# Kernel optimization log

Hardware: AMD Instinct MI355X
Metric: run time of the kernel (lower is better)

Reference implementation:

```python
import jax, jax.numpy as jnp
import numpy as np


def setup_inputs() -> dict:
    key = jax.random.key(0)
    k1, k2 = jax.random.split(key)
    return {
        "embeddings": jax.random.normal(k1, (4, 768, 32, 32), dtype=jnp.float32),
        "database": jax.random.normal(k2, (20000, 768), dtype=jnp.float32),
        "k": 3,
        "out_h": 512,
        "out_w": 512,
    }


def reference(embeddings, database, k, out_h, out_w):
    # embeddings: [B, D, h, w]  (segmenter hidden state), database: [N, D]
    B, D, h, w = embeddings.shape
    # B x h x w x D -> B x (h*w) x D query layout, as in _get_ood_scores
    q = jnp.transpose(embeddings, (0, 2, 3, 1)).reshape(B, h * w, D)
    # squared Euclidean distances via (||q||^2 + ||x||^2 - 2 q.x)
    q2 = jnp.sum(q * q, axis=-1)[..., None]                 # [B, hw, 1]
    x2 = jnp.sum(database * database, axis=-1)[None, None]  # [1, 1, N]
    d2 = q2 + x2 - 2.0 * jnp.einsum("bqd,nd->bqn", q, database)
    dist = jnp.sqrt(jnp.maximum(d2, 1e-12))                 # [B, hw, N]
    # k smallest distances (sklearn kneighbors) then mean over neighbors
    neg_topk, _ = jax.lax.top_k(-dist, k)                   # [B, hw, k]
    ood = jnp.mean(-neg_topk, axis=-1).reshape(B, h, w)
    # F.interpolate(..., mode='bilinear', align_corners=False) == half-pixel bilinear
    ood_up = jax.image.resize(ood[:, None], (B, 1, out_h, out_w), method="bilinear")
    return ood_up
```

## Files before the change

### kernel.cpp

```cpp
#include <hip/hip_runtime.h>
#include <hip/hip_bf16.h>
#include <math.h>

constexpr int B    = 4;
constexpr int D    = 768;
constexpr int HW   = 1024;
constexpr int M    = B * HW;
constexpr int NDB  = 20000;
constexpr int LTP  = 160;
constexpr int OUTH = 512;
constexpr int OUTW = 512;

constexpr int BM     = 512;
constexpr int BN     = 128;
constexpr int KSTEPS = D / 64;
constexpr int NSPLIT = 8;
constexpr int NT     = 40;
constexpr int STEPB  = 128 * 64;

typedef int   i32x8  __attribute__((ext_vector_type(8)));
typedef float f32x16 __attribute__((ext_vector_type(16)));

__device__ __forceinline__ void insert3(float& t0, float& t1, float& t2, float d) {
    float a0 = fminf(d, t0);
    float b0 = fmaxf(d, t0);
    float a1 = fminf(b0, t1);
    float b1 = fmaxf(b0, t1);
    t0 = a0; t1 = a1;
    t2 = fminf(b1, t2);
}

__device__ __forceinline__ unsigned int pack4_fp8(float a, float b, float c, float d) {
    int v = __builtin_amdgcn_cvt_pk_fp8_f32(a, b, 0, false);
    v = __builtin_amdgcn_cvt_pk_fp8_f32(c, d, v, true);
    return (unsigned int)v;
}

__device__ __forceinline__ void gl_lds16(const unsigned char* g, unsigned char* l) {
    __builtin_amdgcn_global_load_lds(
        (const __attribute__((address_space(1))) void*)g,
        (__attribute__((address_space(3))) void*)l, 16, 0, 0);
}

__global__ __launch_bounds__(256) void db_convert(const float* __restrict__ db,
                                                  uint4* __restrict__ dbt8,
                                                  float* __restrict__ x2p) {
    __shared__ float panel[128][68];
    __shared__ float part[512];
    const int lt = blockIdx.x;
    const int g  = blockIdx.y;
    const int t  = threadIdx.x;
    const int n0 = lt * 128;

    #pragma unroll
    for (int pass = 0; pass < 8; ++pass) {
        int idx = pass * 256 + t;
        int row = idx >> 4, c4 = idx & 15;
        int n = n0 + row;
        float4 v = make_float4(0.f, 0.f, 0.f, 0.f);
        if (n < NDB) v = *(const float4*)(db + (size_t)n * D + g * 64 + c4 * 4);
        *(float4*)&panel[row][c4 * 4] = v;
    }
    __syncthreads();
    #pragma unroll
    for (int pass = 0; pass < 2; ++pass) {
        int idx = pass * 256 + t;
        int r  = idx & 31;
        int kc = (idx >> 5) & 1;
        int h2 = (idx >> 6) & 1;
        int rg = idx >> 7;
        int row  = rg * 32 + r;
        int kloc = kc * 32 + h2 * 16;
        float4 va = *(const float4*)&panel[row][kloc + 0];
        float4 vb = *(const float4*)&panel[row][kloc + 4];
        float4 vc = *(const float4*)&panel[row][kloc + 8];
        float4 vd = *(const float4*)&panel[row][kloc + 12];
        float ss = va.x*va.x + va.y*va.y + va.z*va.z + va.w*va.w
                 + vb.x*vb.x + vb.y*vb.y + vb.z*vb.z + vb.w*vb.w
                 + vc.x*vc.x + vc.y*vc.y + vc.z*vc.z + vc.w*vc.w
                 + vd.x*vd.x + vd.y*vd.y + vd.z*vd.z + vd.w*vd.w;
        uint4 o;
        o.x = pack4_fp8(va.x, va.y, va.z, va.w);
        o.y = pack4_fp8(vb.x, vb.y, vb.z, vb.w);
        o.z = pack4_fp8(vc.x, vc.y, vc.z, vc.w);
        o.w = pack4_fp8(vd.x, vd.y, vd.z, vd.w);
        dbt8[((size_t)lt * KSTEPS + g) * 512 + idx] = o;
        part[idx] = ss;
    }
    __syncthreads();
    if (t < 128) {
        int base = (t >> 5) * 128 + (t & 31);
        float s = part[base] + part[base + 32] + part[base + 64] + part[base + 96];
        x2p[((size_t)lt * KSTEPS + g) * 128 + t] = s;
    }
}

__global__ __launch_bounds__(256) void q_convert(const float* __restrict__ emb,
                                                 uint4* __restrict__ qbt8,
                                                 float* __restrict__ q2p) {
    __shared__ float part[512];
    const int qt = blockIdx.x;
    const int g  = blockIdx.y;
    const int t  = threadIdx.x;
    const int b  = qt >> 3;
    const int p0 = (qt & 7) * 128;

    #pragma unroll
    for (int pass = 0; pass < 2; ++pass) {
        int idx = pass * 256 + t;
        int r  = idx & 31;
        int kc = (idx >> 5) & 1;
        int h2 = (idx >> 6) & 1;
        int rg = idx >> 7;
        int prow = rg * 32 + r;
        int kb = g * 64 + kc * 32 + h2 * 16;
        const float* src = emb + ((size_t)b * D + kb) * HW + p0 + prow;
        float v[16];
        float ss = 0.f;
        #pragma unroll
        for (int j = 0; j < 16; ++j) {
            v[j] = src[(size_t)j * HW];
            ss = fmaf(v[j], v[j], ss);
        }
        uint4 o;
        o.x = pack4_fp8(-2.f*v[0],  -2.f*v[1],  -2.f*v[2],  -2.f*v[3]);
        o.y = pack4_fp8(-2.f*v[4],  -2.f*v[5],  -2.f*v[6],  -2.f*v[7]);
        o.z = pack4_fp8(-2.f*v[8],  -2.f*v[9],  -2.f*v[10], -2.f*v[11]);
        o.w = pack4_fp8(-2.f*v[12], -2.f*v[13], -2.f*v[14], -2.f*v[15]);
        qbt8[((size_t)qt * KSTEPS + g) * 512 + idx] = o;
        part[idx] = ss;
    }
    __syncthreads();
    if (t < 128) {
        int base = (t >> 5) * 128 + (t & 31);
        float s = part[base] + part[base + 32] + part[base + 64] + part[base + 96];
        q2p[((size_t)qt * KSTEPS + g) * 128 + t] = s;
    }
}

__global__ __launch_bounds__(512, 2) void gemm_topk(const unsigned char* __restrict__ dbt8,
                                                    const unsigned char* __restrict__ qbt8,
                                                    const float* __restrict__ x2p,
                                                    float* __restrict__ partials) {
    __shared__ __align__(16) unsigned char Bq[KSTEPS * 8192];
    __shared__ float red[8][BN][3];

    const int tid  = threadIdx.x;
    const int lane = tid & 63;
    const int w    = tid >> 6;
    const int h    = lane >> 5;
    const int l31  = lane & 31;

    const int bid   = blockIdx.x;
    const int sp    = bid & 7;
    const int qtile = bid >> 3;
    const int m0    = qtile * BN;

    {
        const unsigned char* qb = qbt8 + (size_t)qtile * KSTEPS * STEPB;
        #pragma unroll
        for (int p = 0; p < 12; ++p) {
            int idx = p * 512 + tid;
            gl_lds16(qb + (size_t)idx * 16, Bq + idx * 16);
        }
    }
    __syncthreads();

    int b_off[4];
    #pragma unroll
    for (int j4 = 0; j4 < 4; ++j4) b_off[j4] = j4 * 2048 + h * 512 + l31 * 16;

    float t0[4], t1[4], t2[4];
    #pragma unroll
    for (int j4 = 0; j4 < 4; ++j4) { t0[j4] = INFINITY; t1[j4] = INFINITY; t2[j4] = INFINITY; }

    const unsigned char* aP = dbt8 + ((size_t)(4 * sp + (w >> 1)) * KSTEPS) * STEPB
                              + (w & 1) * 4096 + h * 512 + l31 * 16;

    auto ldA = [&](i32x8& x0, i32x8& x1, const unsigned char* p) {
        int4 a = *(const int4*)(p);
        int4 b = *(const int4*)(p + 1024);
        int4 c = *(const int4*)(p + 2048);
        int4 d = *(const int4*)(p + 3072);
        x0 = (i32x8){a.x, a.y, a.z, a.w, b.x, b.y, b.z, b.w};
        x1 = (i32x8){c.x, c.y, c.z, c.w, d.x, d.y, d.z, d.w};
    };

    for (int t = sp; t < NT; t += NSPLIT) {
        float sx = 1e30f;
        {
            int n = t * 512 + w * 64 + lane;
            if (n < NDB) {
                const float* p = x2p + (size_t)(n >> 7) * (KSTEPS * 128) + (n & 127);
                sx = 0.f;
                #pragma unroll
                for (int g = 0; g < KSTEPS; ++g) sx += p[g * 128];
            }
        }

        f32x16 acc[2][4];
        #pragma unroll
        for (int i = 0; i < 2; ++i)
            #pragma unroll
            for (int j4 = 0; j4 < 4; ++j4)
                #pragma unroll
                for (int r = 0; r < 16; ++r) acc[i][j4][r] = 0.f;

        i32x8 af0, af1, an0, an1;
        const unsigned char* aPtr = aP;
        ldA(af0, af1, aPtr); aPtr += STEPB;
        #pragma unroll
        for (int g = 0; g < KSTEPS; ++g) {
            if (g + 1 < KSTEPS) { ldA(an0, an1, aPtr); aPtr += STEPB; }
            const unsigned char* Bb = Bq + g * 8192;
            i32x8 bf[4];
            #pragma unroll
            for (int j4 = 0; j4 < 4; ++j4) {
                int4 lo = *(const int4*)(Bb + b_off[j4]);
                int4 hi = *(const int4*)(Bb + b_off[j4] + 1024);
                bf[j4] = (i32x8){lo.x, lo.y, lo.z, lo.w, hi.x, hi.y, hi.z, hi.w};
            }
            __builtin_amdgcn_s_setprio(1);
            #pragma unroll
            for (int j4 = 0; j4 < 4; ++j4) {
                acc[0][j4] = __builtin_amdgcn_mfma_scale_f32_32x32x64_f8f6f4(
                    af0, bf[j4], acc[0][j4], 0, 0, 0, 0x7f7f7f7f, 0, 0x7f7f7f7f);
                acc[1][j4] = __builtin_amdgcn_mfma_scale_f32_32x32x64_f8f6f4(
                    af1, bf[j4], acc[1][j4], 0, 0, 0, 0x7f7f7f7f, 0, 0x7f7f7f7f);
            }
            __builtin_amdgcn_s_setprio(0);
            af0 = an0; af1 = an1;
        }
        aP += (size_t)32 * KSTEPS * STEPB;

        #pragma unroll
        for (int i = 0; i < 2; ++i) {
            #pragma unroll
            for (int rg2 = 0; rg2 < 4; ++rg2) {
                #pragma unroll
                for (int rr = 0; rr < 4; ++rr) {
                    float xv = __shfl(sx, i * 32 + rg2 * 8 + 4 * h + rr);
                    #pragma unroll
                    for (int j4 = 0; j4 < 4; ++j4)
                        insert3(t0[j4], t1[j4], t2[j4], acc[i][j4][rg2 * 4 + rr] + xv);
                }
            }
        }
    }

    #pragma unroll
    for (int j4 = 0; j4 < 4; ++j4) {
        float o0 = __shfl_xor(t0[j4], 32);
        float o1 = __shfl_xor(t1[j4], 32);
        float o2 = __shfl_xor(t2[j4], 32);
        insert3(t0[j4], t1[j4], t2[j4], o0);
        insert3(t0[j4], t1[j4], t2[j4], o1);
        insert3(t0[j4], t1[j4], t2[j4], o2);
    }
    if (h == 0) {
        #pragma unroll
        for (int j4 = 0; j4 < 4; ++j4) {
            int col = j4 * 32 + l31;
            red[w][col][0] = t0[j4];
            red[w][col][1] = t1[j4];
            red[w][col][2] = t2[j4];
        }
    }
    __syncthreads();
    if (tid < BN) {
        float a0 = red[0][tid][0], a1 = red[0][tid][1], a2 = red[0][tid][2];
        #pragma unroll
        for (int ww = 1; ww < 8; ++ww) {
            insert3(a0, a1, a2, red[ww][tid][0]);
            insert3(a0, a1, a2, red[ww][tid][1]);
            insert3(a0, a1, a2, red[ww][tid][2]);
        }
        float* dst = partials + ((size_t)(m0 + tid) * NSPLIT + sp) * 3;
        dst[0] = a0; dst[1] = a1; dst[2] = a2;
    }
}

__global__ __launch_bounds__(256) void merge_ood(const float* __restrict__ partials,
                                                 const float* __restrict__ q2p,
                                                 float* __restrict__ ood) {
    int m = blockIdx.x * 256 + threadIdx.x;
    if (m >= M) return;
    const float* pp = partials + (size_t)m * NSPLIT * 3;
    float a0 = INFINITY, a1 = INFINITY, a2 = INFINITY;
    #pragma unroll
    for (int j = 0; j < NSPLIT * 3; ++j) insert3(a0, a1, a2, pp[j]);
    const float* qp = q2p + (size_t)(m >> 7) * KSTEPS * 128 + (m & 127);
    float q = 0.f;
    #pragma unroll
    for (int g = 0; g < KSTEPS; ++g) q += qp[g * 128];
    float d0 = sqrtf(fmaxf(q + a0, 1e-12f));
    float d1 = sqrtf(fmaxf(q + a1, 1e-12f));
    float d2 = sqrtf(fmaxf(q + a2, 1e-12f));
    ood[m] = (d0 + d1 + d2) * (1.f / 3.f);
}

__global__ __launch_bounds__(256) void upsample(const float* __restrict__ ood,
                                                float* __restrict__ out) {
    int idx = blockIdx.x * 256 + threadIdx.x;
    int ox = idx & (OUTW - 1);
    int oy = (idx >> 9) & (OUTH - 1);
    int bb = idx >> 18;
    float sx = (ox + 0.5f) * (32.f / OUTW) - 0.5f;
    float sy = (oy + 0.5f) * (32.f / OUTH) - 0.5f;
    float fx = floorf(sx), fy = floorf(sy);
    float wx = sx - fx, wy = sy - fy;
    int x0 = max(0, min(31, (int)fx));
    int x1 = max(0, min(31, (int)fx + 1));
    int y0 = max(0, min(31, (int)fy));
    int y1 = max(0, min(31, (int)fy + 1));
    const float* src = ood + bb * 1024;
    float v00 = src[y0 * 32 + x0];
    float v01 = src[y0 * 32 + x1];
    float v10 = src[y1 * 32 + x0];
    float v11 = src[y1 * 32 + x1];
    float top = v00 + wx * (v01 - v00);
    float bot = v10 + wx * (v11 - v10);
    out[idx] = top + wy * (bot - top);
}

extern "C" void kernel_launch(void* const* d_in, const int* in_sizes, int n_in,
                              void* d_out, int out_size, void* d_ws, size_t ws_size,
                              hipStream_t stream) {
    const float* emb = (const float*)d_in[0];
    const float* db  = (const float*)d_in[1];
    float* out = (float*)d_out;

    char* ws = (char*)d_ws;
    unsigned char* dbt8 = (unsigned char*)ws;
    unsigned char* qbt8 = (unsigned char*)(ws + 15728640);
    float* x2p      = (float*)(ws + 18874368);
    float* q2p      = (float*)(ws + 19857408);
    float* ood      = (float*)(ws + 20054016);
    float* partials = (float*)(ws + 20070400);

    db_convert<<<dim3(LTP, KSTEPS), 256, 0, stream>>>(db, (uint4*)dbt8, x2p);
    q_convert<<<dim3(32, KSTEPS), 256, 0, stream>>>(emb, (uint4*)qbt8, q2p);
    gemm_topk<<<NSPLIT * 32, 512, 0, stream>>>(dbt8, qbt8, x2p, partials);
    merge_ood<<<(M + 255) / 256, 256, 0, stream>>>(partials, q2p, ood);
    upsample<<<(B * OUTH * OUTW) / 256, 256, 0, stream>>>(ood, out);
}
```

Baseline: 219.8 us.

## Halve GEMM block size, double split count, and triple-buffer query tiles in LDS

The fused distance GEMM/top-k kernel now uses 256-thread blocks over 256-row database tiles with 16 splits, which doubles the grid to 512 blocks. Blocks are mapped so each XCD handles one split. The full 96 KB query tile is no longer preloaded into LDS. Query K-slices are now streamed through a 3-slot ring buffer with async global-to-LDS loads, with explicit waitcnt/barrier staging interleaved between the MFMA halves. Database tiling is changed to 158 tiles with uneven per-split tile counts. The aim is to raise occupancy, cut LDS footprint and overlap loads with compute, at the cost of many more barriers per K-step.

```diff
diff --git a/kernel.cpp b/kernel.cpp
--- a/kernel.cpp
+++ b/kernel.cpp
@@ -7,15 +7,15 @@
 constexpr int HW   = 1024;
 constexpr int M    = B * HW;
 constexpr int NDB  = 20000;
-constexpr int LTP  = 160;
+constexpr int LT   = 158;
 constexpr int OUTH = 512;
 constexpr int OUTW = 512;
 
-constexpr int BM     = 512;
+constexpr int BM     = 256;
 constexpr int BN     = 128;
 constexpr int KSTEPS = D / 64;
-constexpr int NSPLIT = 8;
-constexpr int NT     = 40;
+constexpr int NSPLIT = 16;
+constexpr int NT2    = 79;
 constexpr int STEPB  = 128 * 64;
 
 typedef int   i32x8  __attribute__((ext_vector_type(8)));
@@ -138,44 +138,38 @@
     }
 }
 
-__global__ __launch_bounds__(512, 2) void gemm_topk(const unsigned char* __restrict__ dbt8,
+__global__ __launch_bounds__(256, 2) void gemm_topk(const unsigned char* __restrict__ dbt8,
                                                     const unsigned char* __restrict__ qbt8,
                                                     const float* __restrict__ x2p,
                                                     float* __restrict__ partials) {
-    __shared__ __align__(16) unsigned char Bq[KSTEPS * 8192];
-    __shared__ float red[8][BN][3];
+    __shared__ __align__(16) unsigned char Bsm[3 * 8192];
+    __shared__ float red[4][BN][3];
 
     const int tid  = threadIdx.x;
     const int lane = tid & 63;
     const int w    = tid >> 6;
+    const int lts  = w >> 1;
+    const int wr   = w & 1;
     const int h    = lane >> 5;
     const int l31  = lane & 31;
 
     const int bid   = blockIdx.x;
-    const int sp    = bid & 7;
-    const int qtile = bid >> 3;
+    const int xcd   = bid & 7;
+    const int j     = bid >> 3;
+    const int sp    = xcd + 8 * (j >> 5);
+    const int qtile = j & 31;
     const int m0    = qtile * BN;
 
-    {
-        const unsigned char* qb = qbt8 + (size_t)qtile * KSTEPS * STEPB;
-        #pragma unroll
-        for (int p = 0; p < 12; ++p) {
-            int idx = p * 512 + tid;
-            gl_lds16(qb + (size_t)idx * 16, Bq + idx * 16);
-        }
-    }
-    __syncthreads();
-
     int b_off[4];
     #pragma unroll
     for (int j4 = 0; j4 < 4; ++j4) b_off[j4] = j4 * 2048 + h * 512 + l31 * 16;
 
-    float t0[4], t1[4], t2[4];
-    #pragma unroll
-    for (int j4 = 0; j4 < 4; ++j4) { t0[j4] = INFINITY; t1[j4] = INFINITY; t2[j4] = INFINITY; }
-
-    const unsigned char* aP = dbt8 + ((size_t)(4 * sp + (w >> 1)) * KSTEPS) * STEPB
-                              + (w & 1) * 4096 + h * 512 + l31 * 16;
+    const int frag = wr * 4096 + h * 512 + l31 * 16;
+
+    const unsigned char* bQ = qbt8 + (size_t)qtile * KSTEPS * STEPB + w * 2048 + lane * 16;
+    unsigned char* bD = Bsm + w * 2048;
+
+    const int ntiles = (sp <= 14) ? 5 : 4;
 
     auto ldA = [&](i32x8& x0, i32x8& x1, const unsigned char* p) {
         int4 a = *(const int4*)(p);
@@ -185,18 +179,42 @@
         x0 = (i32x8){a.x, a.y, a.z, a.w, b.x, b.y, b.z, b.w};
         x1 = (i32x8){c.x, c.y, c.z, c.w, d.x, d.y, d.z, d.w};
     };
-
-    for (int t = sp; t < NT; t += NSPLIT) {
-        float sx = 1e30f;
-        {
-            int n = t * 512 + w * 64 + lane;
-            if (n < NDB) {
-                const float* p = x2p + (size_t)(n >> 7) * (KSTEPS * 128) + (n & 127);
-                sx = 0.f;
-                #pragma unroll
-                for (int g = 0; g < KSTEPS; ++g) sx += p[g * 128];
-            }
-        }
+    auto ldB = [&](i32x8& f, const unsigned char* Bb, int off) {
+        int4 lo = *(const int4*)(Bb + off);
+        int4 hi = *(const int4*)(Bb + off + 1024);
+        f = (i32x8){lo.x, lo.y, lo.z, lo.w, hi.x, hi.y, hi.z, hi.w};
+    };
+
+    gl_lds16(bQ + 0 * STEPB,        bD + 0 * 8192);
+    gl_lds16(bQ + 0 * STEPB + 1024, bD + 0 * 8192 + 1024);
+    const unsigned char* aT = dbt8 + (size_t)(2 * sp + lts) * KSTEPS * STEPB + frag;
+    i32x8 af0, af1, an0, an1;
+    ldA(af0, af1, aT);
+    gl_lds16(bQ + 1 * STEPB,        bD + 1 * 8192);
+    gl_lds16(bQ + 1 * STEPB + 1024, bD + 1 * 8192 + 1024);
+    asm volatile("s_waitcnt vmcnt(6)" ::: "memory");
+    __builtin_amdgcn_sched_barrier(0);
+    __builtin_amdgcn_s_barrier();
+    __builtin_amdgcn_sched_barrier(0);
+
+    float sx = 1e30f;
+    {
+        int n = sp * BM + w * 64 + lane;
+        if (n < NDB) {
+            const float* p = x2p + (size_t)(n >> 7) * (KSTEPS * 128) + (n & 127);
+            sx = 0.f;
+            #pragma unroll
+            for (int g = 0; g < KSTEPS; ++g) sx += p[g * 128];
+        }
+    }
+
+    float t0[4], t1[4], t2[4];
+    #pragma unroll
+    for (int j4 = 0; j4 < 4; ++j4) { t0[j4] = INFINITY; t1[j4] = INFINITY; t2[j4] = INFINITY; }
+
+    for (int tt = 0; tt < ntiles; ++tt) {
+        const unsigned char* aTn = (tt + 1 < ntiles)
+            ? aT + (size_t)2 * NSPLIT * KSTEPS * STEPB : aT;
 
         f32x16 acc[2][4];
         #pragma unroll
@@ -206,32 +224,57 @@
                 #pragma unroll
                 for (int r = 0; r < 16; ++r) acc[i][j4][r] = 0.f;
 
-        i32x8 af0, af1, an0, an1;
-        const unsigned char* aPtr = aP;
-        ldA(af0, af1, aPtr); aPtr += STEPB;
         #pragma unroll
         for (int g = 0; g < KSTEPS; ++g) {
-            if (g + 1 < KSTEPS) { ldA(an0, an1, aPtr); aPtr += STEPB; }
-            const unsigned char* Bb = Bq + g * 8192;
-            i32x8 bf[4];
-            #pragma unroll
-            for (int j4 = 0; j4 < 4; ++j4) {
-                int4 lo = *(const int4*)(Bb + b_off[j4]);
-                int4 hi = *(const int4*)(Bb + b_off[j4] + 1024);
-                bf[j4] = (i32x8){lo.x, lo.y, lo.z, lo.w, hi.x, hi.y, hi.z, hi.w};
-            }
+            const unsigned char* Bb = Bsm + (g % 3) * 8192;
+            const int sb = ((g + 2) % 3) * 8192;
+            const int gs = (g + 2) % KSTEPS;
+
+            i32x8 bf0, bf1;
+            ldB(bf0, Bb, b_off[0]);
+            ldB(bf1, Bb, b_off[1]);
+            { const unsigned char* aLd = (g < KSTEPS - 1) ? (aT + (g + 1) * STEPB) : aTn;
+              ldA(an0, an1, aLd); }
+            asm volatile("s_waitcnt vmcnt(6)" ::: "memory");
+            __builtin_amdgcn_sched_barrier(0);
+            __builtin_amdgcn_s_barrier();
+            __builtin_amdgcn_sched_barrier(0);
+            asm volatile("s_waitcnt lgkmcnt(0)" ::: "memory");
             __builtin_amdgcn_s_setprio(1);
-            #pragma unroll
-            for (int j4 = 0; j4 < 4; ++j4) {
-                acc[0][j4] = __builtin_amdgcn_mfma_scale_f32_32x32x64_f8f6f4(
-                    af0, bf[j4], acc[0][j4], 0, 0, 0, 0x7f7f7f7f, 0, 0x7f7f7f7f);
-                acc[1][j4] = __builtin_amdgcn_mfma_scale_f32_32x32x64_f8f6f4(
-                    af1, bf[j4], acc[1][j4], 0, 0, 0, 0x7f7f7f7f, 0, 0x7f7f7f7f);
-            }
+            acc[0][0] = __builtin_amdgcn_mfma_scale_f32_32x32x64_f8f6f4(
+                af0, bf0, acc[0][0], 0, 0, 0, 0x7f7f7f7f, 0, 0x7f7f7f7f);
+            acc[1][0] = __builtin_amdgcn_mfma_scale_f32_32x32x64_f8f6f4(
+                af1, bf0, acc[1][0], 0, 0, 0, 0x7f7f7f7f, 0, 0x7f7f7f7f);
+            acc[0][1] = __builtin_amdgcn_mfma_scale_f32_32x32x64_f8f6f4(
+                af0, bf1, acc[0][1], 0, 0, 0, 0x7f7f7f7f, 0, 0x7f7f7f7f);
+            acc[1][1] = __builtin_amdgcn_mfma_scale_f32_32x32x64_f8f6f4(
+                af1, bf1, acc[1][1], 0, 0, 0, 0x7f7f7f7f, 0, 0x7f7f7f7f);
             __builtin_amdgcn_s_setprio(0);
+
+            i32x8 bf2, bf3;
+            ldB(bf2, Bb, b_off[2]);
+            ldB(bf3, Bb, b_off[3]);
+            gl_lds16(bQ + gs * STEPB,        bD + sb);
+            gl_lds16(bQ + gs * STEPB + 1024, bD + sb + 1024);
+            asm volatile("s_waitcnt vmcnt(6)" ::: "memory");
+            __builtin_amdgcn_sched_barrier(0);
+            __builtin_amdgcn_s_barrier();
+            __builtin_amdgcn_sched_barrier(0);
+            asm volatile("s_waitcnt lgkmcnt(0)" ::: "memory");
+            __builtin_amdgcn_s_setprio(1);
+            acc[0][2] = __builtin_amdgcn_mfma_scale_f32_32x32x64_f8f6f4(
+                af0, bf2, acc[0][2], 0, 0, 0, 0x7f7f7f7f, 0, 0x7f7f7f7f);
+            acc[1][2] = __builtin_amdgcn_mfma_scale_f32_32x32x64_f8f6f4(
+                af1, bf2, acc[1][2], 0, 0, 0, 0x7f7f7f7f, 0, 0x7f7f7f7f);
+            acc[0][3] = __builtin_amdgcn_mfma_scale_f32_32x32x64_f8f6f4(
+                af0, bf3, acc[0][3], 0, 0, 0, 0x7f7f7f7f, 0, 0x7f7f7f7f);
+            acc[1][3] = __builtin_amdgcn_mfma_scale_f32_32x32x64_f8f6f4(
+                af1, bf3, acc[1][3], 0, 0, 0, 0x7f7f7f7f, 0, 0x7f7f7f7f);
+            __builtin_amdgcn_s_setprio(0);
+
             af0 = an0; af1 = an1;
         }
-        aP += (size_t)32 * KSTEPS * STEPB;
+        aT = aTn;
 
         #pragma unroll
         for (int i = 0; i < 2; ++i) {
@@ -246,6 +289,17 @@
                 }
             }
         }
+
+        if (tt + 1 < ntiles) {
+            int n = (sp + (tt + 1) * NSPLIT) * BM + w * 64 + lane;
+            sx = 1e30f;
+            if (n < NDB) {
+                const float* p = x2p + (size_t)(n >> 7) * (KSTEPS * 128) + (n & 127);
+                sx = 0.f;
+                #pragma unroll
+                for (int g = 0; g < KSTEPS; ++g) sx += p[g * 128];
+            }
+        }
     }
 
     #pragma unroll
@@ -270,7 +324,7 @@
     if (tid < BN) {
         float a0 = red[0][tid][0], a1 = red[0][tid][1], a2 = red[0][tid][2];
         #pragma unroll
-        for (int ww = 1; ww < 8; ++ww) {
+        for (int ww = 1; ww < 4; ++ww) {
             insert3(a0, a1, a2, red[ww][tid][0]);
             insert3(a0, a1, a2, red[ww][tid][1]);
             insert3(a0, a1, a2, red[ww][tid][2]);
@@ -332,15 +386,15 @@
 
     char* ws = (char*)d_ws;
     unsigned char* dbt8 = (unsigned char*)ws;
-    unsigned char* qbt8 = (unsigned char*)(ws + 15728640);
-    float* x2p      = (float*)(ws + 18874368);
-    float* q2p      = (float*)(ws + 19857408);
-    float* ood      = (float*)(ws + 20054016);
-    float* partials = (float*)(ws + 20070400);
-
-    db_convert<<<dim3(LTP, KSTEPS), 256, 0, stream>>>(db, (uint4*)dbt8, x2p);
+    unsigned char* qbt8 = (unsigned char*)(ws + 15532032);
+    float* x2p      = (float*)(ws + 18677760);
+    float* q2p      = (float*)(ws + 19648512);
+    float* ood      = (float*)(ws + 19845120);
+    float* partials = (float*)(ws + 19861504);
+
+    db_convert<<<dim3(LT, KSTEPS), 256, 0, stream>>>(db, (uint4*)dbt8, x2p);
     q_convert<<<dim3(32, KSTEPS), 256, 0, stream>>>(emb, (uint4*)qbt8, q2p);
-    gemm_topk<<<NSPLIT * 32, 512, 0, stream>>>(dbt8, qbt8, x2p, partials);
+    gemm_topk<<<NSPLIT * 32, 256, 0, stream>>>(dbt8, qbt8, x2p, partials);
     merge_ood<<<(M + 255) / 256, 256, 0, stream>>>(partials, q2p, ood);
     upsample<<<(B * OUTH * OUTW) / 256, 256, 0, stream>>>(ood, out);
 }
```

Result: slower. 793.0 us (+260.8%).

## Fuse conversion kernels and double-buffer query tiles in smaller GEMM blocks

Applied to the files above, without the earlier changes.

Merges the database and query fp8 conversion kernels into one launch. Reworks gemm_topk to use 256-thread blocks with a 256-row database tile and 16-way split, launching 512 blocks instead of 256 and mapping splits across XCDs. Instead of staging the whole 96KB query tile in LDS up front, it streams per-k-step query slices into a 16KB double buffer. This adds a barrier each k-step and drops the setprio hints. The intent is lower LDS use, better occupancy and less prologue latency, at the cost of more synchronisation and more query reloads.

```diff
diff --git a/kernel.cpp b/kernel.cpp
--- a/kernel.cpp
+++ b/kernel.cpp
@@ -7,15 +7,15 @@
 constexpr int HW   = 1024;
 constexpr int M    = B * HW;
 constexpr int NDB  = 20000;
-constexpr int LTP  = 160;
+constexpr int LT   = 158;
 constexpr int OUTH = 512;
 constexpr int OUTW = 512;
 
-constexpr int BM     = 512;
+constexpr int BM     = 256;
 constexpr int BN     = 128;
 constexpr int KSTEPS = D / 64;
-constexpr int NSPLIT = 8;
-constexpr int NT     = 40;
+constexpr int NSPLIT = 16;
+constexpr int NT2    = 79;
 constexpr int STEPB  = 128 * 64;
 
 typedef int   i32x8  __attribute__((ext_vector_type(8)));
@@ -42,140 +42,132 @@
         (__attribute__((address_space(3))) void*)l, 16, 0, 0);
 }
 
-__global__ __launch_bounds__(256) void db_convert(const float* __restrict__ db,
-                                                  uint4* __restrict__ dbt8,
-                                                  float* __restrict__ x2p) {
+__global__ __launch_bounds__(256) void convert_all(const float* __restrict__ db,
+                                                   const float* __restrict__ emb,
+                                                   uint4* __restrict__ dbt8,
+                                                   uint4* __restrict__ qbt8,
+                                                   float* __restrict__ x2p,
+                                                   float* __restrict__ q2p) {
     __shared__ float panel[128][68];
     __shared__ float part[512];
-    const int lt = blockIdx.x;
-    const int g  = blockIdx.y;
-    const int t  = threadIdx.x;
-    const int n0 = lt * 128;
-
-    #pragma unroll
-    for (int pass = 0; pass < 8; ++pass) {
-        int idx = pass * 256 + t;
-        int row = idx >> 4, c4 = idx & 15;
-        int n = n0 + row;
-        float4 v = make_float4(0.f, 0.f, 0.f, 0.f);
-        if (n < NDB) v = *(const float4*)(db + (size_t)n * D + g * 64 + c4 * 4);
-        *(float4*)&panel[row][c4 * 4] = v;
-    }
-    __syncthreads();
-    #pragma unroll
-    for (int pass = 0; pass < 2; ++pass) {
-        int idx = pass * 256 + t;
-        int r  = idx & 31;
-        int kc = (idx >> 5) & 1;
-        int h2 = (idx >> 6) & 1;
-        int rg = idx >> 7;
-        int row  = rg * 32 + r;
-        int kloc = kc * 32 + h2 * 16;
-        float4 va = *(const float4*)&panel[row][kloc + 0];
-        float4 vb = *(const float4*)&panel[row][kloc + 4];
-        float4 vc = *(const float4*)&panel[row][kloc + 8];
-        float4 vd = *(const float4*)&panel[row][kloc + 12];
-        float ss = va.x*va.x + va.y*va.y + va.z*va.z + va.w*va.w
-                 + vb.x*vb.x + vb.y*vb.y + vb.z*vb.z + vb.w*vb.w
-                 + vc.x*vc.x + vc.y*vc.y + vc.z*vc.z + vc.w*vc.w
-                 + vd.x*vd.x + vd.y*vd.y + vd.z*vd.z + vd.w*vd.w;
-        uint4 o;
-        o.x = pack4_fp8(va.x, va.y, va.z, va.w);
-        o.y = pack4_fp8(vb.x, vb.y, vb.z, vb.w);
-        o.z = pack4_fp8(vc.x, vc.y, vc.z, vc.w);
-        o.w = pack4_fp8(vd.x, vd.y, vd.z, vd.w);
-        dbt8[((size_t)lt * KSTEPS + g) * 512 + idx] = o;
-        part[idx] = ss;
-    }
-    __syncthreads();
-    if (t < 128) {
-        int base = (t >> 5) * 128 + (t & 31);
-        float s = part[base] + part[base + 32] + part[base + 64] + part[base + 96];
-        x2p[((size_t)lt * KSTEPS + g) * 128 + t] = s;
-    }
-}
-
-__global__ __launch_bounds__(256) void q_convert(const float* __restrict__ emb,
-                                                 uint4* __restrict__ qbt8,
-                                                 float* __restrict__ q2p) {
-    __shared__ float part[512];
-    const int qt = blockIdx.x;
-    const int g  = blockIdx.y;
-    const int t  = threadIdx.x;
-    const int b  = qt >> 3;
-    const int p0 = (qt & 7) * 128;
-
-    #pragma unroll
-    for (int pass = 0; pass < 2; ++pass) {
-        int idx = pass * 256 + t;
-        int r  = idx & 31;
-        int kc = (idx >> 5) & 1;
-        int h2 = (idx >> 6) & 1;
-        int rg = idx >> 7;
-        int prow = rg * 32 + r;
-        int kb = g * 64 + kc * 32 + h2 * 16;
-        const float* src = emb + ((size_t)b * D + kb) * HW + p0 + prow;
-        float v[16];
-        float ss = 0.f;
-        #pragma unroll
-        for (int j = 0; j < 16; ++j) {
-            v[j] = src[(size_t)j * HW];
-            ss = fmaf(v[j], v[j], ss);
-        }
-        uint4 o;
-        o.x = pack4_fp8(-2.f*v[0],  -2.f*v[1],  -2.f*v[2],  -2.f*v[3]);
-        o.y = pack4_fp8(-2.f*v[4],  -2.f*v[5],  -2.f*v[6],  -2.f*v[7]);
-        o.z = pack4_fp8(-2.f*v[8],  -2.f*v[9],  -2.f*v[10], -2.f*v[11]);
-        o.w = pack4_fp8(-2.f*v[12], -2.f*v[13], -2.f*v[14], -2.f*v[15]);
-        qbt8[((size_t)qt * KSTEPS + g) * 512 + idx] = o;
-        part[idx] = ss;
-    }
-    __syncthreads();
-    if (t < 128) {
-        int base = (t >> 5) * 128 + (t & 31);
-        float s = part[base] + part[base + 32] + part[base + 64] + part[base + 96];
-        q2p[((size_t)qt * KSTEPS + g) * 128 + t] = s;
-    }
-}
-
-__global__ __launch_bounds__(512, 2) void gemm_topk(const unsigned char* __restrict__ dbt8,
+    const int g = blockIdx.y;
+    const int t = threadIdx.x;
+
+    if (blockIdx.x < LT) {
+        const int lt = blockIdx.x;
+        const int n0 = lt * 128;
+
+        #pragma unroll
+        for (int pass = 0; pass < 8; ++pass) {
+            int idx = pass * 256 + t;
+            int row = idx >> 4, c4 = idx & 15;
+            int n = n0 + row;
+            float4 v = make_float4(0.f, 0.f, 0.f, 0.f);
+            if (n < NDB) v = *(const float4*)(db + (size_t)n * D + g * 64 + c4 * 4);
+            *(float4*)&panel[row][c4 * 4] = v;
+        }
+        __syncthreads();
+        #pragma unroll
+        for (int pass = 0; pass < 2; ++pass) {
+            int idx = pass * 256 + t;
+            int r  = idx & 31;
+            int kc = (idx >> 5) & 1;
+            int h2 = (idx >> 6) & 1;
+            int rg = idx >> 7;
+            int row  = rg * 32 + r;
+            int kloc = kc * 32 + h2 * 16;
+            float4 va = *(const float4*)&panel[row][kloc + 0];
+            float4 vb = *(const float4*)&panel[row][kloc + 4];
+            float4 vc = *(const float4*)&panel[row][kloc + 8];
+            float4 vd = *(const float4*)&panel[row][kloc + 12];
+            float ss = va.x*va.x + va.y*va.y + va.z*va.z + va.w*va.w
+                     + vb.x*vb.x + vb.y*vb.y + vb.z*vb.z + vb.w*vb.w
+                     + vc.x*vc.x + vc.y*vc.y + vc.z*vc.z + vc.w*vc.w
+                     + vd.x*vd.x + vd.y*vd.y + vd.z*vd.z + vd.w*vd.w;
+            uint4 o;
+            o.x = pack4_fp8(va.x, va.y, va.z, va.w);
+            o.y = pack4_fp8(vb.x, vb.y, vb.z, vb.w);
+            o.z = pack4_fp8(vc.x, vc.y, vc.z, vc.w);
+            o.w = pack4_fp8(vd.x, vd.y, vd.z, vd.w);
+            dbt8[((size_t)lt * KSTEPS + g) * 512 + idx] = o;
+            part[idx] = ss;
+        }
+        __syncthreads();
+        if (t < 128) {
+            int base = (t >> 5) * 128 + (t & 31);
+            float s = part[base] + part[base + 32] + part[base + 64] + part[base + 96];
+            x2p[((size_t)lt * KSTEPS + g) * 128 + t] = s;
+        }
+    } else {
+        const int qt = blockIdx.x - LT;
+        const int b  = qt >> 3;
+        const int p0 = (qt & 7) * 128;
+
+        #pragma unroll
+        for (int pass = 0; pass < 2; ++pass) {
+            int idx = pass * 256 + t;
+            int r  = idx & 31;
+            int kc = (idx >> 5) & 1;
+            int h2 = (idx >> 6) & 1;
+            int rg = idx >> 7;
+            int prow = rg * 32 + r;
+            int kb = g * 64 + kc * 32 + h2 * 16;
+            const float* src = emb + ((size_t)b * D + kb) * HW + p0 + prow;
+            float v[16];
+            float ss = 0.f;
+            #pragma unroll
+            for (int j = 0; j < 16; ++j) {
+                v[j] = src[(size_t)j * HW];
+                ss = fmaf(v[j], v[j], ss);
+            }
+            uint4 o;
+            o.x = pack4_fp8(-2.f*v[0],  -2.f*v[1],  -2.f*v[2],  -2.f*v[3]);
+            o.y = pack4_fp8(-2.f*v[4],  -2.f*v[5],  -2.f*v[6],  -2.f*v[7]);
+            o.z = pack4_fp8(-2.f*v[8],  -2.f*v[9],  -2.f*v[10], -2.f*v[11]);
+            o.w = pack4_fp8(-2.f*v[12], -2.f*v[13], -2.f*v[14], -2.f*v[15]);
+            qbt8[((size_t)qt * KSTEPS + g) * 512 + idx] = o;
+            part[idx] = ss;
+        }
+        __syncthreads();
+        if (t < 128) {
+            int base = (t >> 5) * 128 + (t & 31);
+            float s = part[base] + part[base + 32] + part[base + 64] + part[base + 96];
+            q2p[((size_t)qt * KSTEPS + g) * 128 + t] = s;
+        }
+    }
+}
+
+__global__ __launch_bounds__(256, 2) void gemm_topk(const unsigned char* __restrict__ dbt8,
                                                     const unsigned char* __restrict__ qbt8,
                                                     const float* __restrict__ x2p,
                                                     float* __restrict__ partials) {
-    __shared__ __align__(16) unsigned char Bq[KSTEPS * 8192];
-    __shared__ float red[8][BN][3];
+    __shared__ __align__(16) unsigned char Bsm[2 * 8192];
+    __shared__ float red[4][BN][3];
 
     const int tid  = threadIdx.x;
     const int lane = tid & 63;
     const int w    = tid >> 6;
+    const int lts  = w >> 1;
+    const int wr   = w & 1;
     const int h    = lane >> 5;
     const int l31  = lane & 31;
 
     const int bid   = blockIdx.x;
-    const int sp    = bid & 7;
-    const int qtile = bid >> 3;
+    const int xcd   = bid & 7;
+    const int j     = bid >> 3;
+    const int sp    = xcd + 8 * (j >> 5);
+    const int qtile = j & 31;
     const int m0    = qtile * BN;
 
-    {
-        const unsigned char* qb = qbt8 + (size_t)qtile * KSTEPS * STEPB;
-        #pragma unroll
-        for (int p = 0; p < 12; ++p) {
-            int idx = p * 512 + tid;
-            gl_lds16(qb + (size_t)idx * 16, Bq + idx * 16);
-        }
-    }
-    __syncthreads();
-
     int b_off[4];
     #pragma unroll
     for (int j4 = 0; j4 < 4; ++j4) b_off[j4] = j4 * 2048 + h * 512 + l31 * 16;
 
-    float t0[4], t1[4], t2[4];
-    #pragma unroll
-    for (int j4 = 0; j4 < 4; ++j4) { t0[j4] = INFINITY; t1[j4] = INFINITY; t2[j4] = INFINITY; }
-
-    const unsigned char* aP = dbt8 + ((size_t)(4 * sp + (w >> 1)) * KSTEPS) * STEPB
-                              + (w & 1) * 4096 + h * 512 + l31 * 16;
+    const unsigned char* aT = dbt8 + (size_t)(2 * sp + lts) * KSTEPS * STEPB
+                              + wr * 4096 + h * 512 + l31 * 16;
+
+    const unsigned char* bQ = qbt8 + (size_t)qtile * KSTEPS * STEPB + w * 2048 + lane * 16;
+    unsigned char* bD = Bsm + w * 2048;
 
     auto ldA = [&](i32x8& x0, i32x8& x1, const unsigned char* p) {
         int4 a = *(const int4*)(p);
@@ -185,11 +177,25 @@
         x0 = (i32x8){a.x, a.y, a.z, a.w, b.x, b.y, b.z, b.w};
         x1 = (i32x8){c.x, c.y, c.z, c.w, d.x, d.y, d.z, d.w};
     };
-
-    for (int t = sp; t < NT; t += NSPLIT) {
+    auto ldB = [&](i32x8& f, const unsigned char* Bb, int off) {
+        int4 lo = *(const int4*)(Bb + off);
+        int4 hi = *(const int4*)(Bb + off + 1024);
+        f = (i32x8){lo.x, lo.y, lo.z, lo.w, hi.x, hi.y, hi.z, hi.w};
+    };
+
+    gl_lds16(bQ,        bD);
+    gl_lds16(bQ + 1024, bD + 1024);
+
+    float t0[4], t1[4], t2[4];
+    #pragma unroll
+    for (int j4 = 0; j4 < 4; ++j4) { t0[j4] = INFINITY; t1[j4] = INFINITY; t2[j4] = INFINITY; }
+
+    for (int tile = sp; tile < NT2; tile += NSPLIT) {
+        const bool lastTile = (tile + NSPLIT >= NT2);
+
         float sx = 1e30f;
         {
-            int n = t * 512 + w * 64 + lane;
+            int n = tile * BM + w * 64 + lane;
             if (n < NDB) {
                 const float* p = x2p + (size_t)(n >> 7) * (KSTEPS * 128) + (n & 127);
                 sx = 0.f;
@@ -207,20 +213,27 @@
                 for (int r = 0; r < 16; ++r) acc[i][j4][r] = 0.f;
 
         i32x8 af0, af1, an0, an1;
-        const unsigned char* aPtr = aP;
-        ldA(af0, af1, aPtr); aPtr += STEPB;
-        #pragma unroll
+        ldA(af0, af1, aT);
+
+        #pragma unroll 2
         for (int g = 0; g < KSTEPS; ++g) {
-            if (g + 1 < KSTEPS) { ldA(an0, an1, aPtr); aPtr += STEPB; }
-            const unsigned char* Bb = Bq + g * 8192;
+            __syncthreads();
+
+            if (g + 1 < KSTEPS) {
+                gl_lds16(bQ + (g + 1) * STEPB,        bD + ((g + 1) & 1) * 8192);
+                gl_lds16(bQ + (g + 1) * STEPB + 1024, bD + ((g + 1) & 1) * 8192 + 1024);
+            } else if (!lastTile) {
+                gl_lds16(bQ,        bD);
+                gl_lds16(bQ + 1024, bD + 1024);
+            }
+
+            if (g + 1 < KSTEPS) ldA(an0, an1, aT + (g + 1) * STEPB);
+
+            const unsigned char* Bb = Bsm + (g & 1) * 8192;
             i32x8 bf[4];
             #pragma unroll
-            for (int j4 = 0; j4 < 4; ++j4) {
-                int4 lo = *(const int4*)(Bb + b_off[j4]);
-                int4 hi = *(const int4*)(Bb + b_off[j4] + 1024);
-                bf[j4] = (i32x8){lo.x, lo.y, lo.z, lo.w, hi.x, hi.y, hi.z, hi.w};
-            }
-            __builtin_amdgcn_s_setprio(1);
+            for (int j4 = 0; j4 < 4; ++j4) ldB(bf[j4], Bb, b_off[j4]);
+
             #pragma unroll
             for (int j4 = 0; j4 < 4; ++j4) {
                 acc[0][j4] = __builtin_amdgcn_mfma_scale_f32_32x32x64_f8f6f4(
@@ -228,10 +241,9 @@
                 acc[1][j4] = __builtin_amdgcn_mfma_scale_f32_32x32x64_f8f6f4(
                     af1, bf[j4], acc[1][j4], 0, 0, 0, 0x7f7f7f7f, 0, 0x7f7f7f7f);
             }
-            __builtin_amdgcn_s_setprio(0);
             af0 = an0; af1 = an1;
         }
-        aP += (size_t)32 * KSTEPS * STEPB;
+        aT += (size_t)2 * NSPLIT * KSTEPS * STEPB;
 
         #pragma unroll
         for (int i = 0; i < 2; ++i) {
@@ -270,7 +282,7 @@
     if (tid < BN) {
         float a0 = red[0][tid][0], a1 = red[0][tid][1], a2 = red[0][tid][2];
         #pragma unroll
-        for (int ww = 1; ww < 8; ++ww) {
+        for (int ww = 1; ww < 4; ++ww) {
             insert3(a0, a1, a2, red[ww][tid][0]);
             insert3(a0, a1, a2, red[ww][tid][1]);
             insert3(a0, a1, a2, red[ww][tid][2]);
@@ -332,15 +344,15 @@
 
     char* ws = (char*)d_ws;
     unsigned char* dbt8 = (unsigned char*)ws;
-    unsigned char* qbt8 = (unsigned char*)(ws + 15728640);
-    float* x2p      = (float*)(ws + 18874368);
-    float* q2p      = (float*)(ws + 19857408);
-    float* ood      = (float*)(ws + 20054016);
-    float* partials = (float*)(ws + 20070400);
-
-    db_convert<<<dim3(LTP, KSTEPS), 256, 0, stream>>>(db, (uint4*)dbt8, x2p);
-    q_convert<<<dim3(32, KSTEPS), 256, 0, stream>>>(emb, (uint4*)qbt8, q2p);
-    gemm_topk<<<NSPLIT * 32, 512, 0, stream>>>(dbt8, qbt8, x2p, partials);
+    unsigned char* qbt8 = (unsigned char*)(ws + 15532032);
+    float* x2p      = (float*)(ws + 18677760);
+    float* q2p      = (float*)(ws + 19648512);
+    float* ood      = (float*)(ws + 19845120);
+    float* partials = (float*)(ws + 19861504);
+
+    convert_all<<<dim3(LT + 32, KSTEPS), 256, 0, stream>>>(db, emb, (uint4*)dbt8,
+                                                           (uint4*)qbt8, x2p, q2p);
+    gemm_topk<<<NSPLIT * 32, 256, 0, stream>>>(dbt8, qbt8, x2p, partials);
     merge_ood<<<(M + 255) / 256, 256, 0, stream>>>(partials, q2p, ood);
     upsample<<<(B * OUTH * OUTW) / 256, 256, 0, stream>>>(ood, out);
 }
```

New measurement: 182.5 us. 1.2x faster.
